# Performance work log

Hardware: AMD Instinct MI355X
Metric: run time of the kernel (lower is better)

Reference implementation:

```python
import jax, jax.numpy as jnp
import numpy as np

EMBED_DIM = 1024
NUM_HEADS = 16
HEAD_DIM = EMBED_DIM // NUM_HEADS


def setup_inputs() -> dict:
    key = jax.random.key(0)
    ks = jax.random.split(key, 9)
    B, T, C = 4, 2048, EMBED_DIM
    s = 1.0 / np.sqrt(C)
    x = jax.random.normal(ks[0], (B, T, C), dtype=jnp.float32)
    # Linear weights stored as [in, out] for x @ W + b
    Wq = jax.random.normal(ks[1], (C, C), dtype=jnp.float32) * s
    Wk = jax.random.normal(ks[2], (C, C), dtype=jnp.float32) * s
    Wv = jax.random.normal(ks[3], (C, C), dtype=jnp.float32) * s
    Wo = jax.random.normal(ks[4], (C, C), dtype=jnp.float32) * s
    bq = jax.random.normal(ks[5], (C,), dtype=jnp.float32) * 0.01
    bk = jax.random.normal(ks[6], (C,), dtype=jnp.float32) * 0.01
    bv = jax.random.normal(ks[7], (C,), dtype=jnp.float32) * 0.01
    bo = jax.random.normal(ks[8], (C,), dtype=jnp.float32) * 0.01
    return {"x": x, "Wq": Wq, "bq": bq, "Wk": Wk, "bk": bk,
            "Wv": Wv, "bv": bv, "Wo": Wo, "bo": bo}


def reference(x, Wq, bq, Wk, bk, Wv, bv, Wo, bo):
    B, T, C = x.shape
    H, D = NUM_HEADS, HEAD_DIM
    # QKV projections, reshape to [B, H, T, D]
    def proj(W, b):
        return (x @ W + b).reshape(B, T, H, D).transpose(0, 2, 1, 3)
    Q, K, V = proj(Wq, bq), proj(Wk, bk), proj(Wv, bv)
    # scaled dot-product attention (full [B,H,T,T] scores, as in the original)
    scale = 1.0 / np.sqrt(D).astype(np.float32)
    scores = jnp.einsum('bhqd,bhkd->bhqk', Q, K) * scale
    attn = jax.nn.softmax(scores, axis=-1)
    out = jnp.einsum('bhqk,bhkd->bhqd', attn, V)
    out = out.transpose(0, 2, 1, 3).reshape(B, T, C)
    return out @ Wo + bo
```

## Files before the change

kernel.cpp:

```cpp
#include <hip/hip_runtime.h>
#include <cstdint>
#include <cstddef>

#define MTOK 8192
#define CDIM 1024

typedef __bf16 bf16x8 __attribute__((ext_vector_type(8)));
typedef float  f32x4  __attribute__((ext_vector_type(4)));
typedef float  f32x16 __attribute__((ext_vector_type(16)));
typedef uint32_t u32x4 __attribute__((ext_vector_type(4)));

#define QSCALE 0.18033688011112042f

__device__ __forceinline__ uint16_t f2bf(float f) {
    return __builtin_bit_cast(uint16_t, (__bf16)f);
}
__device__ __forceinline__ uint32_t cvtpk(float lo, float hi) {
    return (uint32_t)__builtin_bit_cast(uint16_t, (__bf16)lo) |
           ((uint32_t)__builtin_bit_cast(uint16_t, (__bf16)hi) << 16);
}

__device__ __forceinline__ void gload_lds16(const uint16_t* g, uint16_t* l) {
    __builtin_amdgcn_global_load_lds((const __attribute__((address_space(1))) void*)g,
                                     (__attribute__((address_space(3))) void*)l, 16, 0, 0);
}

__global__ __launch_bounds__(256) void convert_x_kernel(const float* __restrict__ x,
                                                        uint16_t* __restrict__ xb, int n) {
    int i = (blockIdx.x * 256 + threadIdx.x) * 4;
    int stride = gridDim.x * 256 * 4;
    for (; i < n; i += stride) {
        float4 v = *reinterpret_cast<const float4*>(x + i);
        uint64_t pk = (uint64_t)cvtpk(v.x, v.y) | ((uint64_t)cvtpk(v.z, v.w) << 32);
        *reinterpret_cast<uint64_t*>(xb + i) = pk;
    }
}

__global__ __launch_bounds__(256) void transpose_w_kernel(const float* __restrict__ W0,
                                                          const float* __restrict__ W1,
                                                          const float* __restrict__ W2,
                                                          const float* __restrict__ W3,
                                                          uint16_t* __restrict__ Wt) {
    __shared__ float tile[32][33];
    const float* W = blockIdx.z == 0 ? W0 : blockIdx.z == 1 ? W1 : blockIdx.z == 2 ? W2 : W3;
    uint16_t* out = Wt + (size_t)blockIdx.z * 1024 * 1024;
    int k0 = blockIdx.y * 32, n0 = blockIdx.x * 32;
    int tx = threadIdx.x, ty = threadIdx.y;
#pragma unroll
    for (int i = 0; i < 4; i++) tile[ty * 4 + i][tx] = W[(size_t)(k0 + ty * 4 + i) * 1024 + n0 + tx];
    __syncthreads();
#pragma unroll
    for (int i = 0; i < 4; i++) out[(size_t)(n0 + ty * 4 + i) * 1024 + k0 + tx] = f2bf(tile[tx][ty * 4 + i]);
}

__device__ __forceinline__ void gemm_stage(const uint16_t* __restrict__ A,
                                           const uint16_t* __restrict__ Wt,
                                           int m0, int n0, int k0,
                                           uint16_t* Als, uint16_t* Bls,
                                           int r, int cc, int wave) {
    gload_lds16(A + (size_t)(m0 + r) * 1024 + k0 + cc, Als + wave * 512);
    gload_lds16(A + (size_t)(m0 + 64 + r) * 1024 + k0 + cc, Als + 2048 + wave * 512);
    gload_lds16(Wt + (size_t)(n0 + r) * 1024 + k0 + cc, Bls + wave * 512);
    gload_lds16(Wt + (size_t)(n0 + 64 + r) * 1024 + k0 + cc, Bls + 2048 + wave * 512);
}

__device__ __forceinline__ void gemm128_mainloop(const uint16_t* __restrict__ A,
                                                 const uint16_t* __restrict__ Wt,
                                                 int m0, int n0,
                                                 uint16_t* Als, uint16_t* Bls,
                                                 f32x4 acc[4][4]) {
    const int tid = threadIdx.x;
    const int wave = tid >> 6, lane = tid & 63;
    const int g = lane >> 4, c = lane & 15;
    const int wr = wave >> 1, wc = wave & 1;
    const int r = tid >> 2, cc = (tid & 3) * 8;
#pragma unroll
    for (int mi = 0; mi < 4; mi++)
#pragma unroll
        for (int ni = 0; ni < 4; ni++) acc[mi][ni] = f32x4{0.f, 0.f, 0.f, 0.f};

    gemm_stage(A, Wt, m0, n0, 0, Als, Bls, r, cc, wave);
    __syncthreads();

    int cur = 0;
    for (int k0 = 0; k0 < 1024; k0 += 32, cur ^= 1) {
        if (k0 + 32 < 1024)
            gemm_stage(A, Wt, m0, n0, k0 + 32,
                       Als + (cur ^ 1) * 4096, Bls + (cur ^ 1) * 4096, r, cc, wave);
        const uint16_t* Ab = Als + cur * 4096;
        const uint16_t* Bb = Bls + cur * 4096;
        bf16x8 af[4], bf[4];
#pragma unroll
        for (int mi = 0; mi < 4; mi++)
            af[mi] = *reinterpret_cast<const bf16x8*>(Ab + (wr * 64 + mi * 16 + c) * 32 + g * 8);
#pragma unroll
        for (int ni = 0; ni < 4; ni++)
            bf[ni] = *reinterpret_cast<const bf16x8*>(Bb + (wc * 64 + ni * 16 + c) * 32 + g * 8);
#pragma unroll
        for (int mi = 0; mi < 4; mi++)
#pragma unroll
            for (int ni = 0; ni < 4; ni++)
                acc[mi][ni] = __builtin_amdgcn_mfma_f32_16x16x32_bf16(af[mi], bf[ni], acc[mi][ni], 0, 0, 0);
        __syncthreads();
    }
}

__global__ __launch_bounds__(256) void qkv_gemm_kernel(const uint16_t* __restrict__ xb,
                                                       const uint16_t* __restrict__ WtAll,
                                                       const float* __restrict__ bq,
                                                       const float* __restrict__ bk,
                                                       const float* __restrict__ bv,
                                                       uint16_t* __restrict__ Qg,
                                                       uint16_t* __restrict__ Kg,
                                                       uint16_t* __restrict__ Vtg) {
    __shared__ uint16_t Als[8192], Bls[8192];
    const int z = blockIdx.z;
    const uint16_t* Wt = WtAll + (size_t)z * 1024 * 1024;
    const float* bias = z == 0 ? bq : z == 1 ? bk : bv;
    const int m0 = blockIdx.y * 128, n0 = blockIdx.x * 128;
    f32x4 acc[4][4];
    gemm128_mainloop(xb, Wt, m0, n0, Als, Bls, acc);

    const int tid = threadIdx.x, wave = tid >> 6, lane = tid & 63;
    const int g = lane >> 4, c = lane & 15;
    const int wr = wave >> 1, wc = wave & 1;
#pragma unroll
    for (int ni = 0; ni < 4; ni++) {
        int n = n0 + wc * 64 + ni * 16 + c;
        float bb = bias[n];
        int h = n >> 6, d = n & 63;
#pragma unroll
        for (int mi = 0; mi < 4; mi++)
#pragma unroll
            for (int j = 0; j < 4; j++) {
                int m = m0 + wr * 64 + mi * 16 + g * 4 + j;
                int b = m >> 11, t = m & 2047;
                float v = acc[mi][ni][j] + bb;
                size_t bhOff = (size_t)(b * 16 + h) * 131072;
                if (z == 0)      Qg[bhOff + (size_t)t * 64 + d] = f2bf(v * QSCALE);
                else if (z == 1) Kg[bhOff + (size_t)t * 64 + d] = f2bf(v);
                else             Vtg[bhOff + (size_t)d * 2048 + t] = f2bf(v);
            }
    }
}

__global__ __launch_bounds__(512, 4) void attn_kernel(const uint16_t* __restrict__ Qg,
                                                      const uint16_t* __restrict__ Kg,
                                                      const uint16_t* __restrict__ Vtg,
                                                      uint16_t* __restrict__ Oatt) {
    const int blk = blockIdx.x;
    const int xcd = blk & 7, j = blk >> 3;
    const int bh = xcd * 8 + (j >> 3);
    const int q0 = (j & 7) * 256;

    const int tid = threadIdx.x, wave = tid >> 6, lane = tid & 63;
    const int lo = lane & 31, hi = lane >> 5, lo7 = lo & 7;
    const int qw = q0 + wave * 32;
    const uint16_t* Qb = Qg + (size_t)bh * 131072;
    const uint16_t* Kb = Kg + (size_t)bh * 131072;
    const uint16_t* Vb = Vtg + (size_t)bh * 131072;

    __shared__ __align__(16) uint16_t Kls[2][4096];
    __shared__ __align__(16) uint16_t Vls[2][4096];

    const int sr = lane >> 3;
    const int sc = (lane & 7) ^ (sr & 7);
    const int w8 = wave * 8;

    bf16x8 qf[4];
#pragma unroll
    for (int dc = 0; dc < 4; dc++)
        qf[dc] = *reinterpret_cast<const bf16x8*>(Qb + (size_t)(qw + lo) * 64 + dc * 16 + hi * 8);

    f32x16 o0, o1;
#pragma unroll
    for (int r = 0; r < 16; r++) { o0[r] = 0.f; o1[r] = 0.f; }
    float m = -__builtin_inff(), l = 0.f;

    gload_lds16(Kb + (size_t)(w8 + sr) * 64 + sc * 8, &Kls[0][wave * 512]);
    gload_lds16(Vb + (size_t)(w8 + sr) * 2048 + sc * 8, &Vls[0][wave * 512]);
    __syncthreads();

    for (int t = 0; t < 32; ++t) {
        const int cur = t & 1;
        const uint16_t* Kc = Kls[cur];
        const uint16_t* Vc = Vls[cur];
        if (t < 31) {
            const int kvn = (t + 1) * 64;
            gload_lds16(Kb + (size_t)(kvn + w8 + sr) * 64 + sc * 8, &Kls[cur ^ 1][wave * 512]);
            gload_lds16(Vb + (size_t)(w8 + sr) * 2048 + kvn + sc * 8, &Vls[cur ^ 1][wave * 512]);
        }

        f32x16 p0, p1;
#pragma unroll
        for (int r = 0; r < 16; r++) { p0[r] = 0.f; p1[r] = 0.f; }
        {
            const uint16_t* base = Kc + lo * 64;
            bf16x8 ka = *reinterpret_cast<const bf16x8*>(base + (((0 + hi) ^ lo7) * 8));
            bf16x8 kb2 = *reinterpret_cast<const bf16x8*>(base + (((2 + hi) ^ lo7) * 8));
            bf16x8 kc2 = *reinterpret_cast<const bf16x8*>(base + (((4 + hi) ^ lo7) * 8));
            bf16x8 kd = *reinterpret_cast<const bf16x8*>(base + (((6 + hi) ^ lo7) * 8));
            __builtin_amdgcn_s_setprio(1);
            p0 = __builtin_amdgcn_mfma_f32_32x32x16_bf16(ka, qf[0], p0, 0, 0, 0);
            p0 = __builtin_amdgcn_mfma_f32_32x32x16_bf16(kb2, qf[1], p0, 0, 0, 0);
            p0 = __builtin_amdgcn_mfma_f32_32x32x16_bf16(kc2, qf[2], p0, 0, 0, 0);
            p0 = __builtin_amdgcn_mfma_f32_32x32x16_bf16(kd, qf[3], p0, 0, 0, 0);
            __builtin_amdgcn_s_setprio(0);
        }
        {
            const uint16_t* base = Kc + (32 + lo) * 64;
            bf16x8 ka = *reinterpret_cast<const bf16x8*>(base + (((0 + hi) ^ lo7) * 8));
            bf16x8 kb2 = *reinterpret_cast<const bf16x8*>(base + (((2 + hi) ^ lo7) * 8));
            bf16x8 kc2 = *reinterpret_cast<const bf16x8*>(base + (((4 + hi) ^ lo7) * 8));
            bf16x8 kd = *reinterpret_cast<const bf16x8*>(base + (((6 + hi) ^ lo7) * 8));
            __builtin_amdgcn_s_setprio(1);
            p1 = __builtin_amdgcn_mfma_f32_32x32x16_bf16(ka, qf[0], p1, 0, 0, 0);
            p1 = __builtin_amdgcn_mfma_f32_32x32x16_bf16(kb2, qf[1], p1, 0, 0, 0);
            p1 = __builtin_amdgcn_mfma_f32_32x32x16_bf16(kc2, qf[2], p1, 0, 0, 0);
            p1 = __builtin_amdgcn_mfma_f32_32x32x16_bf16(kd, qf[3], p1, 0, 0, 0);
            __builtin_amdgcn_s_setprio(0);
        }

        float mx[8];
#pragma unroll
        for (int r = 0; r < 8; r++) mx[r] = fmaxf(fmaxf(p0[r], p0[r + 8]), fmaxf(p1[r], p1[r + 8]));
        float pa = fmaxf(fmaxf(mx[0], mx[1]), fmaxf(mx[2], mx[3]));
        float pb = fmaxf(fmaxf(mx[4], mx[5]), fmaxf(mx[6], mx[7]));
        float pm = fmaxf(pa, pb);
        pm = fmaxf(pm, __shfl_xor(pm, 32));

        if (!__all(pm <= m + 8.f)) {
            float nm = fmaxf(m, pm);
            float al = __builtin_amdgcn_exp2f(m - nm);
            l *= al;
#pragma unroll
            for (int r = 0; r < 16; r++) { o0[r] *= al; o1[r] *= al; }
            m = nm;
        }

        float s0 = 0.f, s1 = 0.f, s2 = 0.f, s3 = 0.f;
#pragma unroll
        for (int r = 0; r < 4; r++) {
            p0[r]      = __builtin_amdgcn_exp2f(p0[r] - m);      s0 += p0[r];
            p0[r + 4]  = __builtin_amdgcn_exp2f(p0[r + 4] - m);  s1 += p0[r + 4];
            p0[r + 8]  = __builtin_amdgcn_exp2f(p0[r + 8] - m);  s2 += p0[r + 8];
            p0[r + 12] = __builtin_amdgcn_exp2f(p0[r + 12] - m); s3 += p0[r + 12];
        }
#pragma unroll
        for (int r = 0; r < 4; r++) {
            p1[r]      = __builtin_amdgcn_exp2f(p1[r] - m);      s0 += p1[r];
            p1[r + 4]  = __builtin_amdgcn_exp2f(p1[r + 4] - m);  s1 += p1[r + 4];
            p1[r + 8]  = __builtin_amdgcn_exp2f(p1[r + 8] - m);  s2 += p1[r + 8];
            p1[r + 12] = __builtin_amdgcn_exp2f(p1[r + 12] - m); s3 += p1[r + 12];
        }
        float rs = (s0 + s1) + (s2 + s3);
        rs += __shfl_xor(rs, 32);
        l += rs;

        uint32_t pk0[8], pk1[8];
#pragma unroll
        for (int rp = 0; rp < 8; rp++) {
            pk0[rp] = cvtpk(p0[2 * rp], p0[2 * rp + 1]);
            pk1[rp] = cvtpk(p1[2 * rp], p1[2 * rp + 1]);
        }
        bf16x8 pf[4];
#pragma unroll
        for (int kc = 0; kc < 4; kc++) {
            const uint32_t* pk = (kc >> 1) ? pk1 : pk0;
            const int b0 = (kc & 1) * 4;
            auto sA = __builtin_amdgcn_permlane32_swap(pk[b0 + 0], pk[b0 + 2], false, false);
            auto sB = __builtin_amdgcn_permlane32_swap(pk[b0 + 1], pk[b0 + 3], false, false);
            pf[kc] = __builtin_bit_cast(bf16x8, u32x4{(uint32_t)sA[0], (uint32_t)sB[0],
                                                      (uint32_t)sA[1], (uint32_t)sB[1]});
        }

        {
            const uint16_t* base = Vc + lo * 64;
            bf16x8 va = *reinterpret_cast<const bf16x8*>(base + (((0 + hi) ^ lo7) * 8));
            bf16x8 vb2 = *reinterpret_cast<const bf16x8*>(base + (((2 + hi) ^ lo7) * 8));
            bf16x8 vc2 = *reinterpret_cast<const bf16x8*>(base + (((4 + hi) ^ lo7) * 8));
            bf16x8 vd = *reinterpret_cast<const bf16x8*>(base + (((6 + hi) ^ lo7) * 8));
            __builtin_amdgcn_s_setprio(1);
            o0 = __builtin_amdgcn_mfma_f32_32x32x16_bf16(va, pf[0], o0, 0, 0, 0);
            o0 = __builtin_amdgcn_mfma_f32_32x32x16_bf16(vb2, pf[1], o0, 0, 0, 0);
            o0 = __builtin_amdgcn_mfma_f32_32x32x16_bf16(vc2, pf[2], o0, 0, 0, 0);
            o0 = __builtin_amdgcn_mfma_f32_32x32x16_bf16(vd, pf[3], o0, 0, 0, 0);
            __builtin_amdgcn_s_setprio(0);
        }
        {
            const uint16_t* base = Vc + (32 + lo) * 64;
            bf16x8 va = *reinterpret_cast<const bf16x8*>(base + (((0 + hi) ^ lo7) * 8));
            bf16x8 vb2 = *reinterpret_cast<const bf16x8*>(base + (((2 + hi) ^ lo7) * 8));
            bf16x8 vc2 = *reinterpret_cast<const bf16x8*>(base + (((4 + hi) ^ lo7) * 8));
            bf16x8 vd = *reinterpret_cast<const bf16x8*>(base + (((6 + hi) ^ lo7) * 8));
            __builtin_amdgcn_s_setprio(1);
            o1 = __builtin_amdgcn_mfma_f32_32x32x16_bf16(va, pf[0], o1, 0, 0, 0);
            o1 = __builtin_amdgcn_mfma_f32_32x32x16_bf16(vb2, pf[1], o1, 0, 0, 0);
            o1 = __builtin_amdgcn_mfma_f32_32x32x16_bf16(vc2, pf[2], o1, 0, 0, 0);
            o1 = __builtin_amdgcn_mfma_f32_32x32x16_bf16(vd, pf[3], o1, 0, 0, 0);
            __builtin_amdgcn_s_setprio(0);
        }

        __syncthreads();
    }

    const int b = bh >> 4, h = bh & 15;
    float inv = 1.0f / l;
    uint16_t* orow = Oatt + (size_t)(b * 2048 + qw + lo) * 1024 + h * 64;
#pragma unroll
    for (int dt = 0; dt < 2; dt++) {
#pragma unroll
        for (int rg = 0; rg < 4; rg++) {
            int dbase = dt * 32 + rg * 8 + hi * 4;
            float v0 = (dt ? o1[rg * 4 + 0] : o0[rg * 4 + 0]) * inv;
            float v1 = (dt ? o1[rg * 4 + 1] : o0[rg * 4 + 1]) * inv;
            float v2 = (dt ? o1[rg * 4 + 2] : o0[rg * 4 + 2]) * inv;
            float v3 = (dt ? o1[rg * 4 + 3] : o0[rg * 4 + 3]) * inv;
            uint2 val;
            val.x = cvtpk(v0, v1);
            val.y = cvtpk(v2, v3);
            *reinterpret_cast<uint2*>(orow + dbase) = val;
        }
    }
}

__global__ __launch_bounds__(256) void out_gemm_kernel(const uint16_t* __restrict__ Oatt,
                                                       const uint16_t* __restrict__ WtO,
                                                       const float* __restrict__ bo,
                                                       float* __restrict__ out) {
    __shared__ uint16_t Als[8192], Bls[8192];
    const int m0 = blockIdx.y * 128, n0 = blockIdx.x * 128;
    f32x4 acc[4][4];
    gemm128_mainloop(Oatt, WtO, m0, n0, Als, Bls, acc);

    const int tid = threadIdx.x, wave = tid >> 6, lane = tid & 63;
    const int g = lane >> 4, c = lane & 15;
    const int wr = wave >> 1, wc = wave & 1;
#pragma unroll
    for (int ni = 0; ni < 4; ni++) {
        int n = n0 + wc * 64 + ni * 16 + c;
        float bb = bo[n];
#pragma unroll
        for (int mi = 0; mi < 4; mi++)
#pragma unroll
            for (int j = 0; j < 4; j++) {
                int m = m0 + wr * 64 + mi * 16 + g * 4 + j;
                out[(size_t)m * 1024 + n] = acc[mi][ni][j] + bb;
            }
    }
}

extern "C" void kernel_launch(void* const* d_in, const int* in_sizes, int n_in,
                              void* d_out, int out_size, void* d_ws, size_t ws_size,
                              hipStream_t stream) {
    const float* x  = (const float*)d_in[0];
    const float* Wq = (const float*)d_in[1];
    const float* bq = (const float*)d_in[2];
    const float* Wk = (const float*)d_in[3];
    const float* bk = (const float*)d_in[4];
    const float* Wv = (const float*)d_in[5];
    const float* bv = (const float*)d_in[6];
    const float* Wo = (const float*)d_in[7];
    const float* bo = (const float*)d_in[8];
    float* out = (float*)d_out;

    char* ws = (char*)d_ws;
    uint16_t* xb   = (uint16_t*)(ws);
    uint16_t* Wt   = (uint16_t*)(ws + 16777216);
    uint16_t* Qg   = (uint16_t*)(ws + 25165824);
    uint16_t* Kg   = (uint16_t*)(ws + 41943040);
    uint16_t* Vtg  = (uint16_t*)(ws + 58720256);
    uint16_t* Oatt = (uint16_t*)(ws);

    convert_x_kernel<<<4096, 256, 0, stream>>>(x, xb, MTOK * CDIM);
    transpose_w_kernel<<<dim3(32, 32, 4), dim3(32, 8), 0, stream>>>(Wq, Wk, Wv, Wo, Wt);
    qkv_gemm_kernel<<<dim3(8, 64, 3), 256, 0, stream>>>(xb, Wt, bq, bk, bv, Qg, Kg, Vtg);
    attn_kernel<<<512, 512, 0, stream>>>(Qg, Kg, Vtg, Oatt);
    out_gemm_kernel<<<dim3(8, 64), 256, 0, stream>>>(Oatt, Wt + (size_t)3 * 1048576, bo, out);
}
```

Baseline: 320.5 us.

## Process two 32-query tiles per wave in attention to reuse K/V fragments

Each attention wave now computes 64 query rows as two independent 32-row tiles, each with its own online-softmax state. Every K and V fragment loaded from LDS is used by two MFMAs, and the two chains are interleaved for instruction-level parallelism. Blocks cover 512 queries, halving the grid to 256 blocks, and launch bounds drop to 2 blocks per CU. This trades lower occupancy and higher register pressure for less LDS traffic per FLOP and fewer redundant K/V tile loads.

```diff
diff --git a/kernel.cpp b/kernel.cpp
--- a/kernel.cpp
+++ b/kernel.cpp
@@ -144,18 +144,18 @@
     }
 }
 
-__global__ __launch_bounds__(512, 4) void attn_kernel(const uint16_t* __restrict__ Qg,
+__global__ __launch_bounds__(512, 2) void attn_kernel(const uint16_t* __restrict__ Qg,
                                                       const uint16_t* __restrict__ Kg,
                                                       const uint16_t* __restrict__ Vtg,
                                                       uint16_t* __restrict__ Oatt) {
     const int blk = blockIdx.x;
     const int xcd = blk & 7, j = blk >> 3;
-    const int bh = xcd * 8 + (j >> 3);
-    const int q0 = (j & 7) * 256;
+    const int bh = xcd * 8 + (j >> 2);
+    const int q0 = (j & 3) * 512;
 
     const int tid = threadIdx.x, wave = tid >> 6, lane = tid & 63;
     const int lo = lane & 31, hi = lane >> 5, lo7 = lo & 7;
-    const int qw = q0 + wave * 32;
+    const int qw = q0 + wave * 64;
     const uint16_t* Qb = Qg + (size_t)bh * 131072;
     const uint16_t* Kb = Kg + (size_t)bh * 131072;
     const uint16_t* Vb = Vtg + (size_t)bh * 131072;
@@ -167,15 +167,18 @@
     const int sc = (lane & 7) ^ (sr & 7);
     const int w8 = wave * 8;
 
-    bf16x8 qf[4];
-#pragma unroll
-    for (int dc = 0; dc < 4; dc++)
-        qf[dc] = *reinterpret_cast<const bf16x8*>(Qb + (size_t)(qw + lo) * 64 + dc * 16 + hi * 8);
-
-    f32x16 o0, o1;
-#pragma unroll
-    for (int r = 0; r < 16; r++) { o0[r] = 0.f; o1[r] = 0.f; }
-    float m = -__builtin_inff(), l = 0.f;
+    bf16x8 qfA[4], qfB[4];
+#pragma unroll
+    for (int dc = 0; dc < 4; dc++) {
+        qfA[dc] = *reinterpret_cast<const bf16x8*>(Qb + (size_t)(qw + lo) * 64 + dc * 16 + hi * 8);
+        qfB[dc] = *reinterpret_cast<const bf16x8*>(Qb + (size_t)(qw + 32 + lo) * 64 + dc * 16 + hi * 8);
+    }
+
+    f32x16 oA0, oA1, oB0, oB1;
+#pragma unroll
+    for (int r = 0; r < 16; r++) { oA0[r] = 0.f; oA1[r] = 0.f; oB0[r] = 0.f; oB1[r] = 0.f; }
+    float mA = -__builtin_inff(), lA = 0.f;
+    float mB = -__builtin_inff(), lB = 0.f;
 
     gload_lds16(Kb + (size_t)(w8 + sr) * 64 + sc * 8, &Kls[0][wave * 512]);
     gload_lds16(Vb + (size_t)(w8 + sr) * 2048 + sc * 8, &Vls[0][wave * 512]);
@@ -191,9 +194,9 @@
             gload_lds16(Vb + (size_t)(w8 + sr) * 2048 + kvn + sc * 8, &Vls[cur ^ 1][wave * 512]);
         }
 
-        f32x16 p0, p1;
-#pragma unroll
-        for (int r = 0; r < 16; r++) { p0[r] = 0.f; p1[r] = 0.f; }
+        f32x16 pA0, pA1, pB0, pB1;
+#pragma unroll
+        for (int r = 0; r < 16; r++) { pA0[r] = 0.f; pA1[r] = 0.f; pB0[r] = 0.f; pB1[r] = 0.f; }
         {
             const uint16_t* base = Kc + lo * 64;
             bf16x8 ka = *reinterpret_cast<const bf16x8*>(base + (((0 + hi) ^ lo7) * 8));
@@ -201,10 +204,14 @@
             bf16x8 kc2 = *reinterpret_cast<const bf16x8*>(base + (((4 + hi) ^ lo7) * 8));
             bf16x8 kd = *reinterpret_cast<const bf16x8*>(base + (((6 + hi) ^ lo7) * 8));
             __builtin_amdgcn_s_setprio(1);
-            p0 = __builtin_amdgcn_mfma_f32_32x32x16_bf16(ka, qf[0], p0, 0, 0, 0);
-            p0 = __builtin_amdgcn_mfma_f32_32x32x16_bf16(kb2, qf[1], p0, 0, 0, 0);
-            p0 = __builtin_amdgcn_mfma_f32_32x32x16_bf16(kc2, qf[2], p0, 0, 0, 0);
-            p0 = __builtin_amdgcn_mfma_f32_32x32x16_bf16(kd, qf[3], p0, 0, 0, 0);
+            pA0 = __builtin_amdgcn_mfma_f32_32x32x16_bf16(ka, qfA[0], pA0, 0, 0, 0);
+            pB0 = __builtin_amdgcn_mfma_f32_32x32x16_bf16(ka, qfB[0], pB0, 0, 0, 0);
+            pA0 = __builtin_amdgcn_mfma_f32_32x32x16_bf16(kb2, qfA[1], pA0, 0, 0, 0);
+            pB0 = __builtin_amdgcn_mfma_f32_32x32x16_bf16(kb2, qfB[1], pB0, 0, 0, 0);
+            pA0 = __builtin_amdgcn_mfma_f32_32x32x16_bf16(kc2, qfA[2], pA0, 0, 0, 0);
+            pB0 = __builtin_amdgcn_mfma_f32_32x32x16_bf16(kc2, qfB[2], pB0, 0, 0, 0);
+            pA0 = __builtin_amdgcn_mfma_f32_32x32x16_bf16(kd, qfA[3], pA0, 0, 0, 0);
+            pB0 = __builtin_amdgcn_mfma_f32_32x32x16_bf16(kd, qfB[3], pB0, 0, 0, 0);
             __builtin_amdgcn_s_setprio(0);
         }
         {
@@ -214,64 +221,117 @@
             bf16x8 kc2 = *reinterpret_cast<const bf16x8*>(base + (((4 + hi) ^ lo7) * 8));
             bf16x8 kd = *reinterpret_cast<const bf16x8*>(base + (((6 + hi) ^ lo7) * 8));
             __builtin_amdgcn_s_setprio(1);
-            p1 = __builtin_amdgcn_mfma_f32_32x32x16_bf16(ka, qf[0], p1, 0, 0, 0);
-            p1 = __builtin_amdgcn_mfma_f32_32x32x16_bf16(kb2, qf[1], p1, 0, 0, 0);
-            p1 = __builtin_amdgcn_mfma_f32_32x32x16_bf16(kc2, qf[2], p1, 0, 0, 0);
-            p1 = __builtin_amdgcn_mfma_f32_32x32x16_bf16(kd, qf[3], p1, 0, 0, 0);
+            pA1 = __builtin_amdgcn_mfma_f32_32x32x16_bf16(ka, qfA[0], pA1, 0, 0, 0);
+            pB1 = __builtin_amdgcn_mfma_f32_32x32x16_bf16(ka, qfB[0], pB1, 0, 0, 0);
+            pA1 = __builtin_amdgcn_mfma_f32_32x32x16_bf16(kb2, qfA[1], pA1, 0, 0, 0);
+            pB1 = __builtin_amdgcn_mfma_f32_32x32x16_bf16(kb2, qfB[1], pB1, 0, 0, 0);
+            pA1 = __builtin_amdgcn_mfma_f32_32x32x16_bf16(kc2, qfA[2], pA1, 0, 0, 0);
+            pB1 = __builtin_amdgcn_mfma_f32_32x32x16_bf16(kc2, qfB[2], pB1, 0, 0, 0);
+            pA1 = __builtin_amdgcn_mfma_f32_32x32x16_bf16(kd, qfA[3], pA1, 0, 0, 0);
+            pB1 = __builtin_amdgcn_mfma_f32_32x32x16_bf16(kd, qfB[3], pB1, 0, 0, 0);
             __builtin_amdgcn_s_setprio(0);
         }
 
-        float mx[8];
-#pragma unroll
-        for (int r = 0; r < 8; r++) mx[r] = fmaxf(fmaxf(p0[r], p0[r + 8]), fmaxf(p1[r], p1[r + 8]));
-        float pa = fmaxf(fmaxf(mx[0], mx[1]), fmaxf(mx[2], mx[3]));
-        float pb = fmaxf(fmaxf(mx[4], mx[5]), fmaxf(mx[6], mx[7]));
-        float pm = fmaxf(pa, pb);
-        pm = fmaxf(pm, __shfl_xor(pm, 32));
-
-        if (!__all(pm <= m + 8.f)) {
-            float nm = fmaxf(m, pm);
-            float al = __builtin_amdgcn_exp2f(m - nm);
-            l *= al;
-#pragma unroll
-            for (int r = 0; r < 16; r++) { o0[r] *= al; o1[r] *= al; }
-            m = nm;
-        }
-
-        float s0 = 0.f, s1 = 0.f, s2 = 0.f, s3 = 0.f;
-#pragma unroll
-        for (int r = 0; r < 4; r++) {
-            p0[r]      = __builtin_amdgcn_exp2f(p0[r] - m);      s0 += p0[r];
-            p0[r + 4]  = __builtin_amdgcn_exp2f(p0[r + 4] - m);  s1 += p0[r + 4];
-            p0[r + 8]  = __builtin_amdgcn_exp2f(p0[r + 8] - m);  s2 += p0[r + 8];
-            p0[r + 12] = __builtin_amdgcn_exp2f(p0[r + 12] - m); s3 += p0[r + 12];
-        }
-#pragma unroll
-        for (int r = 0; r < 4; r++) {
-            p1[r]      = __builtin_amdgcn_exp2f(p1[r] - m);      s0 += p1[r];
-            p1[r + 4]  = __builtin_amdgcn_exp2f(p1[r + 4] - m);  s1 += p1[r + 4];
-            p1[r + 8]  = __builtin_amdgcn_exp2f(p1[r + 8] - m);  s2 += p1[r + 8];
-            p1[r + 12] = __builtin_amdgcn_exp2f(p1[r + 12] - m); s3 += p1[r + 12];
-        }
-        float rs = (s0 + s1) + (s2 + s3);
-        rs += __shfl_xor(rs, 32);
-        l += rs;
-
-        uint32_t pk0[8], pk1[8];
-#pragma unroll
-        for (int rp = 0; rp < 8; rp++) {
-            pk0[rp] = cvtpk(p0[2 * rp], p0[2 * rp + 1]);
-            pk1[rp] = cvtpk(p1[2 * rp], p1[2 * rp + 1]);
-        }
-        bf16x8 pf[4];
-#pragma unroll
-        for (int kc = 0; kc < 4; kc++) {
-            const uint32_t* pk = (kc >> 1) ? pk1 : pk0;
-            const int b0 = (kc & 1) * 4;
-            auto sA = __builtin_amdgcn_permlane32_swap(pk[b0 + 0], pk[b0 + 2], false, false);
-            auto sB = __builtin_amdgcn_permlane32_swap(pk[b0 + 1], pk[b0 + 3], false, false);
-            pf[kc] = __builtin_bit_cast(bf16x8, u32x4{(uint32_t)sA[0], (uint32_t)sB[0],
-                                                      (uint32_t)sA[1], (uint32_t)sB[1]});
+        bf16x8 pfA[4], pfB[4];
+        {
+            float mx[8];
+#pragma unroll
+            for (int r = 0; r < 8; r++) mx[r] = fmaxf(fmaxf(pA0[r], pA0[r + 8]), fmaxf(pA1[r], pA1[r + 8]));
+            float pa = fmaxf(fmaxf(mx[0], mx[1]), fmaxf(mx[2], mx[3]));
+            float pb = fmaxf(fmaxf(mx[4], mx[5]), fmaxf(mx[6], mx[7]));
+            float pm = fmaxf(pa, pb);
+            pm = fmaxf(pm, __shfl_xor(pm, 32));
+            if (!__all(pm <= mA + 8.f)) {
+                float nm = fmaxf(mA, pm);
+                float al = __builtin_amdgcn_exp2f(mA - nm);
+                lA *= al;
+#pragma unroll
+                for (int r = 0; r < 16; r++) { oA0[r] *= al; oA1[r] *= al; }
+                mA = nm;
+            }
+            float s0 = 0.f, s1 = 0.f, s2 = 0.f, s3 = 0.f;
+#pragma unroll
+            for (int r = 0; r < 4; r++) {
+                pA0[r]      = __builtin_amdgcn_exp2f(pA0[r] - mA);      s0 += pA0[r];
+                pA0[r + 4]  = __builtin_amdgcn_exp2f(pA0[r + 4] - mA);  s1 += pA0[r + 4];
+                pA0[r + 8]  = __builtin_amdgcn_exp2f(pA0[r + 8] - mA);  s2 += pA0[r + 8];
+                pA0[r + 12] = __builtin_amdgcn_exp2f(pA0[r + 12] - mA); s3 += pA0[r + 12];
+            }
+#pragma unroll
+            for (int r = 0; r < 4; r++) {
+                pA1[r]      = __builtin_amdgcn_exp2f(pA1[r] - mA);      s0 += pA1[r];
+                pA1[r + 4]  = __builtin_amdgcn_exp2f(pA1[r + 4] - mA);  s1 += pA1[r + 4];
+                pA1[r + 8]  = __builtin_amdgcn_exp2f(pA1[r + 8] - mA);  s2 += pA1[r + 8];
+                pA1[r + 12] = __builtin_amdgcn_exp2f(pA1[r + 12] - mA); s3 += pA1[r + 12];
+            }
+            float rs = (s0 + s1) + (s2 + s3);
+            rs += __shfl_xor(rs, 32);
+            lA += rs;
+            uint32_t pk0[8], pk1[8];
+#pragma unroll
+            for (int rp = 0; rp < 8; rp++) {
+                pk0[rp] = cvtpk(pA0[2 * rp], pA0[2 * rp + 1]);
+                pk1[rp] = cvtpk(pA1[2 * rp], pA1[2 * rp + 1]);
+            }
+#pragma unroll
+            for (int kc = 0; kc < 4; kc++) {
+                const uint32_t* pk = (kc >> 1) ? pk1 : pk0;
+                const int b0 = (kc & 1) * 4;
+                auto sA2 = __builtin_amdgcn_permlane32_swap(pk[b0 + 0], pk[b0 + 2], false, false);
+                auto sB2 = __builtin_amdgcn_permlane32_swap(pk[b0 + 1], pk[b0 + 3], false, false);
+                pfA[kc] = __builtin_bit_cast(bf16x8, u32x4{(uint32_t)sA2[0], (uint32_t)sB2[0],
+                                                           (uint32_t)sA2[1], (uint32_t)sB2[1]});
+            }
+        }
+        {
+            float mx[8];
+#pragma unroll
+            for (int r = 0; r < 8; r++) mx[r] = fmaxf(fmaxf(pB0[r], pB0[r + 8]), fmaxf(pB1[r], pB1[r + 8]));
+            float pa = fmaxf(fmaxf(mx[0], mx[1]), fmaxf(mx[2], mx[3]));
+            float pb = fmaxf(fmaxf(mx[4], mx[5]), fmaxf(mx[6], mx[7]));
+            float pm = fmaxf(pa, pb);
+            pm = fmaxf(pm, __shfl_xor(pm, 32));
+            if (!__all(pm <= mB + 8.f)) {
+                float nm = fmaxf(mB, pm);
+                float al = __builtin_amdgcn_exp2f(mB - nm);
+                lB *= al;
+#pragma unroll
+                for (int r = 0; r < 16; r++) { oB0[r] *= al; oB1[r] *= al; }
+                mB = nm;
+            }
+            float s0 = 0.f, s1 = 0.f, s2 = 0.f, s3 = 0.f;
+#pragma unroll
+            for (int r = 0; r < 4; r++) {
+                pB0[r]      = __builtin_amdgcn_exp2f(pB0[r] - mB);      s0 += pB0[r];
+                pB0[r + 4]  = __builtin_amdgcn_exp2f(pB0[r + 4] - mB);  s1 += pB0[r + 4];
+                pB0[r + 8]  = __builtin_amdgcn_exp2f(pB0[r + 8] - mB);  s2 += pB0[r + 8];
+                pB0[r + 12] = __builtin_amdgcn_exp2f(pB0[r + 12] - mB); s3 += pB0[r + 12];
+            }
+#pragma unroll
+            for (int r = 0; r < 4; r++) {
+                pB1[r]      = __builtin_amdgcn_exp2f(pB1[r] - mB);      s0 += pB1[r];
+                pB1[r + 4]  = __builtin_amdgcn_exp2f(pB1[r + 4] - mB);  s1 += pB1[r + 4];
+                pB1[r + 8]  = __builtin_amdgcn_exp2f(pB1[r + 8] - mB);  s2 += pB1[r + 8];
+                pB1[r + 12] = __builtin_amdgcn_exp2f(pB1[r + 12] - mB); s3 += pB1[r + 12];
+            }
+            float rs = (s0 + s1) + (s2 + s3);
+            rs += __shfl_xor(rs, 32);
+            lB += rs;
+            uint32_t pk0[8], pk1[8];
+#pragma unroll
+            for (int rp = 0; rp < 8; rp++) {
+                pk0[rp] = cvtpk(pB0[2 * rp], pB0[2 * rp + 1]);
+                pk1[rp] = cvtpk(pB1[2 * rp], pB1[2 * rp + 1]);
+            }
+#pragma unroll
+            for (int kc = 0; kc < 4; kc++) {
+                const uint32_t* pk = (kc >> 1) ? pk1 : pk0;
+                const int b0 = (kc & 1) * 4;
+                auto sA2 = __builtin_amdgcn_permlane32_swap(pk[b0 + 0], pk[b0 + 2], false, false);
+                auto sB2 = __builtin_amdgcn_permlane32_swap(pk[b0 + 1], pk[b0 + 3], false, false);
+                pfB[kc] = __builtin_bit_cast(bf16x8, u32x4{(uint32_t)sA2[0], (uint32_t)sB2[0],
+                                                           (uint32_t)sA2[1], (uint32_t)sB2[1]});
+            }
         }
 
         {
@@ -281,10 +341,14 @@
             bf16x8 vc2 = *reinterpret_cast<const bf16x8*>(base + (((4 + hi) ^ lo7) * 8));
             bf16x8 vd = *reinterpret_cast<const bf16x8*>(base + (((6 + hi) ^ lo7) * 8));
             __builtin_amdgcn_s_setprio(1);
-            o0 = __builtin_amdgcn_mfma_f32_32x32x16_bf16(va, pf[0], o0, 0, 0, 0);
-            o0 = __builtin_amdgcn_mfma_f32_32x32x16_bf16(vb2, pf[1], o0, 0, 0, 0);
-            o0 = __builtin_amdgcn_mfma_f32_32x32x16_bf16(vc2, pf[2], o0, 0, 0, 0);
-            o0 = __builtin_amdgcn_mfma_f32_32x32x16_bf16(vd, pf[3], o0, 0, 0, 0);
+            oA0 = __builtin_amdgcn_mfma_f32_32x32x16_bf16(va, pfA[0], oA0, 0, 0, 0);
+            oB0 = __builtin_amdgcn_mfma_f32_32x32x16_bf16(va, pfB[0], oB0, 0, 0, 0);
+            oA0 = __builtin_amdgcn_mfma_f32_32x32x16_bf16(vb2, pfA[1], oA0, 0, 0, 0);
+            oB0 = __builtin_amdgcn_mfma_f32_32x32x16_bf16(vb2, pfB[1], oB0, 0, 0, 0);
+            oA0 = __builtin_amdgcn_mfma_f32_32x32x16_bf16(vc2, pfA[2], oA0, 0, 0, 0);
+            oB0 = __builtin_amdgcn_mfma_f32_32x32x16_bf16(vc2, pfB[2], oB0, 0, 0, 0);
+            oA0 = __builtin_amdgcn_mfma_f32_32x32x16_bf16(vd, pfA[3], oA0, 0, 0, 0);
+            oB0 = __builtin_amdgcn_mfma_f32_32x32x16_bf16(vd, pfB[3], oB0, 0, 0, 0);
             __builtin_amdgcn_s_setprio(0);
         }
         {
@@ -294,10 +358,14 @@
             bf16x8 vc2 = *reinterpret_cast<const bf16x8*>(base + (((4 + hi) ^ lo7) * 8));
             bf16x8 vd = *reinterpret_cast<const bf16x8*>(base + (((6 + hi) ^ lo7) * 8));
             __builtin_amdgcn_s_setprio(1);
-            o1 = __builtin_amdgcn_mfma_f32_32x32x16_bf16(va, pf[0], o1, 0, 0, 0);
-            o1 = __builtin_amdgcn_mfma_f32_32x32x16_bf16(vb2, pf[1], o1, 0, 0, 0);
-            o1 = __builtin_amdgcn_mfma_f32_32x32x16_bf16(vc2, pf[2], o1, 0, 0, 0);
-            o1 = __builtin_amdgcn_mfma_f32_32x32x16_bf16(vd, pf[3], o1, 0, 0, 0);
+            oA1 = __builtin_amdgcn_mfma_f32_32x32x16_bf16(va, pfA[0], oA1, 0, 0, 0);
+            oB1 = __builtin_amdgcn_mfma_f32_32x32x16_bf16(va, pfB[0], oB1, 0, 0, 0);
+            oA1 = __builtin_amdgcn_mfma_f32_32x32x16_bf16(vb2, pfA[1], oA1, 0, 0, 0);
+            oB1 = __builtin_amdgcn_mfma_f32_32x32x16_bf16(vb2, pfB[1], oB1, 0, 0, 0);
+            oA1 = __builtin_amdgcn_mfma_f32_32x32x16_bf16(vc2, pfA[2], oA1, 0, 0, 0);
+            oB1 = __builtin_amdgcn_mfma_f32_32x32x16_bf16(vc2, pfB[2], oB1, 0, 0, 0);
+            oA1 = __builtin_amdgcn_mfma_f32_32x32x16_bf16(vd, pfA[3], oA1, 0, 0, 0);
+            oB1 = __builtin_amdgcn_mfma_f32_32x32x16_bf16(vd, pfB[3], oB1, 0, 0, 0);
             __builtin_amdgcn_s_setprio(0);
         }
 
@@ -305,21 +373,42 @@
     }
 
     const int b = bh >> 4, h = bh & 15;
-    float inv = 1.0f / l;
-    uint16_t* orow = Oatt + (size_t)(b * 2048 + qw + lo) * 1024 + h * 64;
-#pragma unroll
-    for (int dt = 0; dt < 2; dt++) {
-#pragma unroll
-        for (int rg = 0; rg < 4; rg++) {
-            int dbase = dt * 32 + rg * 8 + hi * 4;
-            float v0 = (dt ? o1[rg * 4 + 0] : o0[rg * 4 + 0]) * inv;
-            float v1 = (dt ? o1[rg * 4 + 1] : o0[rg * 4 + 1]) * inv;
-            float v2 = (dt ? o1[rg * 4 + 2] : o0[rg * 4 + 2]) * inv;
-            float v3 = (dt ? o1[rg * 4 + 3] : o0[rg * 4 + 3]) * inv;
-            uint2 val;
-            val.x = cvtpk(v0, v1);
-            val.y = cvtpk(v2, v3);
-            *reinterpret_cast<uint2*>(orow + dbase) = val;
+    {
+        float inv = 1.0f / lA;
+        uint16_t* orow = Oatt + (size_t)(b * 2048 + qw + lo) * 1024 + h * 64;
+#pragma unroll
+        for (int dt = 0; dt < 2; dt++) {
+#pragma unroll
+            for (int rg = 0; rg < 4; rg++) {
+                int dbase = dt * 32 + rg * 8 + hi * 4;
+                float v0 = (dt ? oA1[rg * 4 + 0] : oA0[rg * 4 + 0]) * inv;
+                float v1 = (dt ? oA1[rg * 4 + 1] : oA0[rg * 4 + 1]) * inv;
+                float v2 = (dt ? oA1[rg * 4 + 2] : oA0[rg * 4 + 2]) * inv;
+                float v3 = (dt ? oA1[rg * 4 + 3] : oA0[rg * 4 + 3]) * inv;
+                uint2 val;
+                val.x = cvtpk(v0, v1);
+                val.y = cvtpk(v2, v3);
+                *reinterpret_cast<uint2*>(orow + dbase) = val;
+            }
+        }
+    }
+    {
+        float inv = 1.0f / lB;
+        uint16_t* orow = Oatt + (size_t)(b * 2048 + qw + 32 + lo) * 1024 + h * 64;
+#pragma unroll
+        for (int dt = 0; dt < 2; dt++) {
+#pragma unroll
+            for (int rg = 0; rg < 4; rg++) {
+                int dbase = dt * 32 + rg * 8 + hi * 4;
+                float v0 = (dt ? oB1[rg * 4 + 0] : oB0[rg * 4 + 0]) * inv;
+                float v1 = (dt ? oB1[rg * 4 + 1] : oB0[rg * 4 + 1]) * inv;
+                float v2 = (dt ? oB1[rg * 4 + 2] : oB0[rg * 4 + 2]) * inv;
+                float v3 = (dt ? oB1[rg * 4 + 3] : oB0[rg * 4 + 3]) * inv;
+                uint2 val;
+                val.x = cvtpk(v0, v1);
+                val.y = cvtpk(v2, v3);
+                *reinterpret_cast<uint2*>(orow + dbase) = val;
+            }
         }
     }
 }
@@ -375,6 +464,6 @@
     convert_x_kernel<<<4096, 256, 0, stream>>>(x, xb, MTOK * CDIM);
     transpose_w_kernel<<<dim3(32, 32, 4), dim3(32, 8), 0, stream>>>(Wq, Wk, Wv, Wo, Wt);
     qkv_gemm_kernel<<<dim3(8, 64, 3), 256, 0, stream>>>(xb, Wt, bq, bk, bv, Qg, Kg, Vtg);
-    attn_kernel<<<512, 512, 0, stream>>>(Qg, Kg, Vtg, Oatt);
+    attn_kernel<<<256, 512, 0, stream>>>(Qg, Kg, Vtg, Oatt);
     out_gemm_kernel<<<dim3(8, 64), 256, 0, stream>>>(Oatt, Wt + (size_t)3 * 1048576, bo, out);
 }
```

New measurement: 327.5 us. +2.2%, slower.
